# Optimization experiments

Measured on AMD Instinct MI355X. Metric: run time of the kernel, lower is better.

The kernel has to match this reference:

```python
import jax, jax.numpy as jnp
import numpy as np

B, S, D, H = 2, 2048, 768, 12
DK = D // H


def setup_inputs() -> dict:
    key = jax.random.key(0)
    ks = jax.random.split(key, 12)
    inp = {
        "q": jax.random.normal(ks[0], (B, S, D), jnp.float32),
        "k": jax.random.normal(ks[1], (B, S, D), jnp.float32),
        "v": jax.random.normal(ks[2], (B, S, D), jnp.float32),
        # float mask: 1.0 where attention is disallowed (causal upper triangle)
        "mask": (1.0 - jnp.tril(jnp.ones((S, S), jnp.float32)))[None, None],
        "Wq": jax.random.normal(ks[3], (D, D), jnp.float32) / np.sqrt(D),
        "bq": jnp.zeros((D,), jnp.float32),
        "Wk": jax.random.normal(ks[4], (D, D), jnp.float32) / np.sqrt(D),
        "bk": jnp.zeros((D,), jnp.float32),
        "Wv": jax.random.normal(ks[5], (D, D), jnp.float32) / np.sqrt(D),
        "bv": jnp.zeros((D,), jnp.float32),
        "Wo": jax.random.normal(ks[6], (D, D), jnp.float32) / np.sqrt(D),
        "bo": jnp.zeros((D,), jnp.float32),
    }
    return inp


def _split_heads(x):
    # [B,S,D] -> [B,H,S,DK]
    b, s, _ = x.shape
    return x.reshape(b, s, H, DK).transpose(0, 2, 1, 3)


def reference(q, k, v, mask, Wq, bq, Wk, bk, Wv, bv, Wo, bo):
    Q = _split_heads(q @ Wq + bq)
    K = _split_heads(k @ Wk + bk)
    V = _split_heads(v @ Wv + bv)
    scale = jax.lax.rsqrt(jnp.float32(D))  # note: d_model, not d_k (faithful)
    logits = jnp.einsum("bhqd,bhkd->bhqk", Q, K) * scale
    logits = logits + (-1e9) * mask
    weights = jax.nn.softmax(logits, axis=-1)
    attn = jnp.einsum("bhqk,bhkd->bhqd", weights, V)
    attn = attn.transpose(0, 2, 1, 3).reshape(q.shape)  # [B,S,D]
    return jax.nn.relu(attn @ Wo + bo)
```

## Files before the change

### kernel.cpp

```cpp
#include <hip/hip_runtime.h>
#include <math.h>

#define BB 2
#define SS 2048
#define DD 768
#define HH 12
#define DKK 64
#define MM (BB*SS)

typedef _Float16 half_t;
using half8 = __attribute__((ext_vector_type(8))) _Float16;
using half4 = __attribute__((ext_vector_type(4))) _Float16;
using floatx4 = __attribute__((ext_vector_type(4))) float;

__global__ __launch_bounds__(256)
void prep(const float* __restrict__ q, const float* __restrict__ k,
          const float* __restrict__ v,
          const float* __restrict__ Wq, const float* __restrict__ Wk,
          const float* __restrict__ Wv, const float* __restrict__ Wo,
          half_t* __restrict__ qh, half_t* __restrict__ kh,
          half_t* __restrict__ vh,
          half_t* __restrict__ Wqt, half_t* __restrict__ Wkt,
          half_t* __restrict__ Wvt, half_t* __restrict__ Wot)
{
    __shared__ float tile[64][68];
    const int y = blockIdx.y;
    const int t = threadIdx.x;
    if (y < 3) {
        const float* src = y == 0 ? q : (y == 1 ? k : v);
        half_t* dst      = y == 0 ? qh : (y == 1 ? kh : vh);
        int i = blockIdx.x * 256 + t;
        float4 f = ((const float4*)src)[i];
        half4 hv;
        hv[0] = (half_t)f.x; hv[1] = (half_t)f.y;
        hv[2] = (half_t)f.z; hv[3] = (half_t)f.w;
        ((half4*)dst)[i] = hv;
    } else {
        int x = blockIdx.x;
        if (x >= 576) return;
        int w = x / 144, rem = x % 144;
        const float* W = w == 0 ? Wq : w == 1 ? Wk : w == 2 ? Wv : Wo;
        half_t* T      = w == 0 ? Wqt : w == 1 ? Wkt : w == 2 ? Wvt : Wot;
        int k0 = (rem % 12) * 64, n0 = (rem / 12) * 64;
        #pragma unroll
        for (int i = 0; i < 4; ++i) {
            int c = t + i * 256;
            int kr = c >> 4, nc = (c & 15) * 4;
            *(float4*)&tile[kr][nc] = *(const float4*)&W[(size_t)(k0 + kr) * DD + n0 + nc];
        }
        __syncthreads();
        #pragma unroll
        for (int i = 0; i < 4; ++i) {
            int c = t + i * 256;
            int nr = c >> 4, kc = (c & 15) * 4;
            half4 hv;
            #pragma unroll
            for (int jj = 0; jj < 4; ++jj) hv[jj] = (half_t)tile[kc + jj][nr];
            *(half4*)&T[(size_t)(n0 + nr) * DD + k0 + kc] = hv;
        }
    }
}

template<bool SWAP>
__device__ __forceinline__
void gemm_body(const half_t* __restrict__ A, const half_t* __restrict__ Bt,
               floatx4 (&acc)[4][2], half_t (*As)[72], half_t (*Bs)[72],
               int m0, int n0)
{
    const int t = threadIdx.x;
    const int lane = t & 63, wave = t >> 6;
    const int lr = lane & 15, lq = lane >> 4;
    const int wm = (wave >> 1) * 64, wn = (wave & 1) * 32;
    const int a_r = t >> 1,  a_c = (t & 1) * 32;
    const int b_r = t >> 2,  b_c = (t & 3) * 16;

    #pragma unroll
    for (int mi = 0; mi < 4; ++mi)
        #pragma unroll
        for (int ni = 0; ni < 2; ++ni)
            #pragma unroll
            for (int r = 0; r < 4; ++r) acc[mi][ni][r] = 0.f;

    for (int k0 = 0; k0 < DD; k0 += 64) {
        __syncthreads();
        #pragma unroll
        for (int jj = 0; jj < 4; ++jj)
            *(half8*)&As[a_r][a_c + jj * 8] =
                *(const half8*)&A[(size_t)(m0 + a_r) * DD + k0 + a_c + jj * 8];
        #pragma unroll
        for (int jj = 0; jj < 2; ++jj)
            *(half8*)&Bs[b_r][b_c + jj * 8] =
                *(const half8*)&Bt[(size_t)(n0 + b_r) * DD + k0 + b_c + jj * 8];
        __syncthreads();

        half8 af[4][2], bf[2][2];
        #pragma unroll
        for (int mi = 0; mi < 4; ++mi)
            #pragma unroll
            for (int kp = 0; kp < 2; ++kp)
                af[mi][kp] = *(const half8*)&As[wm + mi * 16 + lr][kp * 32 + lq * 8];
        #pragma unroll
        for (int ni = 0; ni < 2; ++ni)
            #pragma unroll
            for (int kp = 0; kp < 2; ++kp)
                bf[ni][kp] = *(const half8*)&Bs[wn + ni * 16 + lr][kp * 32 + lq * 8];

        #pragma unroll
        for (int mi = 0; mi < 4; ++mi)
            #pragma unroll
            for (int ni = 0; ni < 2; ++ni)
                #pragma unroll
                for (int kp = 0; kp < 2; ++kp) {
                    if (SWAP)
                        acc[mi][ni] = __builtin_amdgcn_mfma_f32_16x16x32_f16(
                            bf[ni][kp], af[mi][kp], acc[mi][ni], 0, 0, 0);
                    else
                        acc[mi][ni] = __builtin_amdgcn_mfma_f32_16x16x32_f16(
                            af[mi][kp], bf[ni][kp], acc[mi][ni], 0, 0, 0);
                }
    }
}

__global__ __launch_bounds__(256)
void proj_gemm(const half_t* __restrict__ qh, const half_t* __restrict__ kh,
               const half_t* __restrict__ vh,
               const half_t* __restrict__ Wqt, const half_t* __restrict__ Wkt,
               const half_t* __restrict__ Wvt,
               const float* __restrict__ bq, const float* __restrict__ bk,
               const float* __restrict__ bv,
               half_t* __restrict__ Qo, half_t* __restrict__ Ko,
               half_t* __restrict__ Vto)
{
    const int z = blockIdx.z;
    const half_t* A  = z == 0 ? qh  : z == 1 ? kh  : vh;
    const half_t* Bt = z == 0 ? Wqt : z == 1 ? Wkt : Wvt;
    const float* bias = z == 0 ? bq : z == 1 ? bk : bv;

    __shared__ half_t As[128][72];
    __shared__ half_t Bs[64][72];
    floatx4 acc[4][2];
    const int m0 = blockIdx.y * 128, n0 = blockIdx.x * 64;

    if (z == 2) gemm_body<true >(A, Bt, acc, As, Bs, m0, n0);
    else        gemm_body<false>(A, Bt, acc, As, Bs, m0, n0);

    const int lane = threadIdx.x & 63, wave = threadIdx.x >> 6;
    const int lr = lane & 15, lq = lane >> 4;
    const int wm = (wave >> 1) * 64, wn = (wave & 1) * 32;

    if (z == 2) {
        #pragma unroll
        for (int mi = 0; mi < 4; ++mi)
            #pragma unroll
            for (int ni = 0; ni < 2; ++ni)
                #pragma unroll
                for (int r = 0; r < 4; ++r) {
                    int dcol = n0 + wn + ni * 16 + lq * 4 + r;
                    int srow = m0 + wm + mi * 16 + lr;
                    int hh = dcol >> 6, d = dcol & 63;
                    int b2 = srow >> 11, sdx = srow & 2047;
                    Vto[((size_t)((b2 * HH + hh) * DKK + d)) * SS + sdx] =
                        (half_t)(acc[mi][ni][r] + bias[dcol]);
                }
    } else {
        const float sc = (z == 0) ? 0.03608439182435161f : 1.0f;
        half_t* O = z == 0 ? Qo : Ko;
        #pragma unroll
        for (int mi = 0; mi < 4; ++mi)
            #pragma unroll
            for (int ni = 0; ni < 2; ++ni)
                #pragma unroll
                for (int r = 0; r < 4; ++r) {
                    int row = m0 + wm + mi * 16 + lq * 4 + r;
                    int col = n0 + wn + ni * 16 + lr;
                    O[(size_t)row * DD + col] = (half_t)((acc[mi][ni][r] + bias[col]) * sc);
                }
    }
}

__global__ __launch_bounds__(256)
void out_gemm(const half_t* __restrict__ A, const half_t* __restrict__ Bt,
              const float* __restrict__ bias, float* __restrict__ C)
{
    __shared__ half_t As[128][72];
    __shared__ half_t Bs[64][72];
    floatx4 acc[4][2];
    const int m0 = blockIdx.y * 128, n0 = blockIdx.x * 64;
    gemm_body<false>(A, Bt, acc, As, Bs, m0, n0);

    const int lane = threadIdx.x & 63, wave = threadIdx.x >> 6;
    const int lr = lane & 15, lq = lane >> 4;
    const int wm = (wave >> 1) * 64, wn = (wave & 1) * 32;

    #pragma unroll
    for (int mi = 0; mi < 4; ++mi)
        #pragma unroll
        for (int ni = 0; ni < 2; ++ni)
            #pragma unroll
            for (int r = 0; r < 4; ++r) {
                int row = m0 + wm + mi * 16 + lq * 4 + r;
                int col = n0 + wn + ni * 16 + lr;
                C[(size_t)row * DD + col] = fmaxf(acc[mi][ni][r] + bias[col], 0.f);
            }
}

__device__ const int QT_TAB[40] = {3,4,5,6,7,7,8,8,9,9,10,10,11,11,11,12,12,12,
                                   13,13,13,14,14,14,15,15,15,15,
                                   2,6,10,14, 1,5,9,13, 0,4,8,12};
__device__ const int C_TAB[40]  = {0,0,0,0,0,1,0,1,0,1,0,1,0,1,2,0,1,2,
                                   0,1,2,0,1,2,0,1,2,3,
                                   0,1,2,3, 0,1,2,3, 0,1,2,3};

__global__ __launch_bounds__(256)
void attn_split(const half_t* __restrict__ Qf, const half_t* __restrict__ Kf,
                const half_t* __restrict__ Vt, half_t* __restrict__ Of,
                float* __restrict__ Opart, float* __restrict__ Lpart)
{
    __shared__ half_t Ks[64][72];
    __shared__ half_t Vs[64][72];
    __shared__ half_t Ps[4][32][72];

    const int i = blockIdx.x;
    const int bh = i % 24;
    const int j = i / 24;
    const int qt = QT_TAB[j];
    const int c  = C_TAB[j];
    const bool single = (qt <= 3);
    const int kt0 = c * 8;
    const int iters = 2 * qt + 2;
    const int kt1 = (kt0 + 8 < iters) ? (kt0 + 8) : iters;

    const int b = bh / HH, h = bh % HH;
    const int t = threadIdx.x;
    const int lane = t & 63, wave = t >> 6;
    const int lr = lane & 15, lq = lane >> 4;
    const int q0 = qt * 128;

    const int srow = t >> 3;
    const int scol = (t & 7) * 8;

    const half_t* Kbase = Kf + (size_t)(b * SS) * DD + h * DKK;
    const half_t* Vbase = Vt + (size_t)((b * HH + h) * DKK) * SS;

    half8 kpre[2], vpre[2];
    #pragma unroll
    for (int ii = 0; ii < 2; ++ii) {
        int row = srow + ii * 32;
        kpre[ii] = *(const half8*)&Kbase[(size_t)(kt0 * 64 + row) * DD + scol];
        vpre[ii] = *(const half8*)&Vbase[(size_t)row * SS + kt0 * 64 + scol];
    }

    half8 qa[2][2];
    #pragma unroll
    for (int qg = 0; qg < 2; ++qg) {
        const half_t* qptr =
            Qf + (size_t)(b * SS + q0 + wave * 32 + qg * 16 + lr) * DD + h * DKK;
        qa[qg][0] = *(const half8*)(qptr + lq * 8);
        qa[qg][1] = *(const half8*)(qptr + 32 + lq * 8);
    }

    floatx4 o[2][4];
    #pragma unroll
    for (int qg = 0; qg < 2; ++qg)
        #pragma unroll
        for (int nt = 0; nt < 4; ++nt)
            #pragma unroll
            for (int r = 0; r < 4; ++r) o[qg][nt][r] = 0.f;
    float l_run[2] = {0.f, 0.f};

    for (int kt = kt0; kt < kt1; ++kt) {
        __syncthreads();
        #pragma unroll
        for (int ii = 0; ii < 2; ++ii) {
            int row = srow + ii * 32;
            *(half8*)&Ks[row][scol] = kpre[ii];
            *(half8*)&Vs[row][scol] = vpre[ii];
        }
        __syncthreads();

        if (kt + 1 < kt1) {
            #pragma unroll
            for (int ii = 0; ii < 2; ++ii) {
                int row = srow + ii * 32;
                kpre[ii] = *(const half8*)&Kbase[(size_t)((kt + 1) * 64 + row) * DD + scol];
                vpre[ii] = *(const half8*)&Vbase[(size_t)row * SS + (kt + 1) * 64 + scol];
            }
        }

        floatx4 s[2][4];
        #pragma unroll
        for (int nt = 0; nt < 4; ++nt) {
            half8 kf0 = *(const half8*)&Ks[nt * 16 + lr][lq * 8];
            half8 kf1 = *(const half8*)&Ks[nt * 16 + lr][32 + lq * 8];
            #pragma unroll
            for (int qg = 0; qg < 2; ++qg) {
                floatx4 a = {0.f, 0.f, 0.f, 0.f};
                a = __builtin_amdgcn_mfma_f32_16x16x32_f16(kf0, qa[qg][0], a, 0, 0, 0);
                a = __builtin_amdgcn_mfma_f32_16x16x32_f16(kf1, qa[qg][1], a, 0, 0, 0);
                s[qg][nt] = a;
            }
        }

        if (kt >= 2 * qt) {
            #pragma unroll
            for (int qg = 0; qg < 2; ++qg) {
                int qrow = q0 + wave * 32 + qg * 16 + lr;
                #pragma unroll
                for (int nt = 0; nt < 4; ++nt)
                    #pragma unroll
                    for (int r = 0; r < 4; ++r) {
                        int key = kt * 64 + nt * 16 + lq * 4 + r;
                        if (key > qrow) s[qg][nt][r] = -1e30f;
                    }
            }
        }

        #pragma unroll
        for (int qg = 0; qg < 2; ++qg)
            #pragma unroll
            for (int nt = 0; nt < 4; ++nt) {
                half4 hp;
                #pragma unroll
                for (int r = 0; r < 4; ++r) {
                    float p = __expf(s[qg][nt][r]);
                    l_run[qg] += p;
                    hp[r] = (half_t)p;
                }
                *(half4*)&Ps[wave][qg * 16 + lr][nt * 16 + lq * 4] = hp;
            }

        __builtin_amdgcn_s_waitcnt(0xc07f);

        half8 pa[2][2];
        #pragma unroll
        for (int qg = 0; qg < 2; ++qg) {
            pa[qg][0] = *(const half8*)&Ps[wave][qg * 16 + lr][lq * 8];
            pa[qg][1] = *(const half8*)&Ps[wave][qg * 16 + lr][32 + lq * 8];
        }

        #pragma unroll
        for (int nt = 0; nt < 4; ++nt) {
            half8 vf0 = *(const half8*)&Vs[nt * 16 + lr][lq * 8];
            half8 vf1 = *(const half8*)&Vs[nt * 16 + lr][32 + lq * 8];
            #pragma unroll
            for (int qg = 0; qg < 2; ++qg) {
                o[qg][nt] = __builtin_amdgcn_mfma_f32_16x16x32_f16(vf0, pa[qg][0], o[qg][nt], 0, 0, 0);
                o[qg][nt] = __builtin_amdgcn_mfma_f32_16x16x32_f16(vf1, pa[qg][1], o[qg][nt], 0, 0, 0);
            }
        }
    }

    #pragma unroll
    for (int qg = 0; qg < 2; ++qg) {
        l_run[qg] += __shfl_xor(l_run[qg], 16);
        l_run[qg] += __shfl_xor(l_run[qg], 32);
    }

    if (single) {
        #pragma unroll
        for (int qg = 0; qg < 2; ++qg) {
            float inv = 1.f / l_run[qg];
            int qrow = q0 + wave * 32 + qg * 16 + lr;
            #pragma unroll
            for (int nt = 0; nt < 4; ++nt) {
                half4 hv;
                #pragma unroll
                for (int r = 0; r < 4; ++r) hv[r] = (half_t)(o[qg][nt][r] * inv);
                *(half4*)&Of[(size_t)(b * SS + qrow) * DD + h * DKK + nt * 16 + lq * 4] = hv;
            }
        }
    } else {
        const int p = (bh * 12 + (qt - 4)) * 4 + c;
        float* Ob = Opart + (size_t)p * 8192;
        #pragma unroll
        for (int qg = 0; qg < 2; ++qg) {
            int qq = wave * 32 + qg * 16 + lr;
            #pragma unroll
            for (int nt = 0; nt < 4; ++nt)
                *(floatx4*)&Ob[qq * 64 + nt * 16 + lq * 4] = o[qg][nt];
            if (lq == 0) Lpart[p * 128 + qq] = l_run[qg];
        }
    }
}

__global__ __launch_bounds__(256)
void attn_combine(const float* __restrict__ Opart, const float* __restrict__ Lpart,
                  half_t* __restrict__ Of)
{
    const int ib = blockIdx.x;
    const int bh = ib / 12, qtm = ib % 12;
    const int qt = qtm + 4;
    const int nc = (2 * qt + 9) / 8;
    const int b = bh / HH, h = bh % HH;
    const int pbase = (bh * 12 + qtm) * 4;
    const int t = threadIdx.x;
    const int qq = t >> 1, ds0 = (t & 1) * 32;

    float l = 0.f;
    for (int cc = 0; cc < nc; ++cc) l += Lpart[(pbase + cc) * 128 + qq];
    const float inv = 1.f / l;

    float4 acc[8];
    #pragma unroll
    for (int kk = 0; kk < 8; ++kk) acc[kk] = make_float4(0.f, 0.f, 0.f, 0.f);
    for (int cc = 0; cc < nc; ++cc) {
        const float* Ob = Opart + (size_t)(pbase + cc) * 8192 + qq * 64 + ds0;
        #pragma unroll
        for (int kk = 0; kk < 8; ++kk) {
            float4 x = *(const float4*)&Ob[kk * 4];
            acc[kk].x += x.x; acc[kk].y += x.y; acc[kk].z += x.z; acc[kk].w += x.w;
        }
    }

    int srow = qt * 128 + qq;
    half_t* dst = Of + (size_t)(b * SS + srow) * DD + h * DKK + ds0;
    #pragma unroll
    for (int kk = 0; kk < 8; ++kk) {
        half4 hv;
        hv[0] = (half_t)(acc[kk].x * inv);
        hv[1] = (half_t)(acc[kk].y * inv);
        hv[2] = (half_t)(acc[kk].z * inv);
        hv[3] = (half_t)(acc[kk].w * inv);
        *(half4*)&dst[kk * 4] = hv;
    }
}

extern "C" void kernel_launch(void* const* d_in, const int* in_sizes, int n_in,
                              void* d_out, int out_size, void* d_ws, size_t ws_size,
                              hipStream_t stream)
{
    (void)in_sizes; (void)n_in; (void)out_size; (void)ws_size;
    const float* q  = (const float*)d_in[0];
    const float* k  = (const float*)d_in[1];
    const float* v  = (const float*)d_in[2];
    const float* Wq = (const float*)d_in[4];
    const float* bq = (const float*)d_in[5];
    const float* Wk = (const float*)d_in[6];
    const float* bk = (const float*)d_in[7];
    const float* Wv = (const float*)d_in[8];
    const float* bv = (const float*)d_in[9];
    const float* Wo = (const float*)d_in[10];
    const float* bo = (const float*)d_in[11];
    float* out = (float*)d_out;

    half_t* qh  = (half_t*)d_ws;
    half_t* kh  = qh  + (size_t)MM * DD;
    half_t* vh  = kh  + (size_t)MM * DD;
    half_t* Wqt = vh  + (size_t)MM * DD;
    half_t* Wkt = Wqt + (size_t)DD * DD;
    half_t* Wvt = Wkt + (size_t)DD * DD;
    half_t* Wot = Wvt + (size_t)DD * DD;
    half_t* Qo  = Wot + (size_t)DD * DD;
    half_t* Ko  = Qo  + (size_t)MM * DD;
    half_t* Vto = Ko  + (size_t)MM * DD;
    half_t* Ao  = Vto + (size_t)MM * DD;
    float* Opart = (float*)(Ao + (size_t)MM * DD);
    float* Lpart = Opart + (size_t)1152 * 8192;

    prep<<<dim3(3072, 4), 256, 0, stream>>>(q, k, v, Wq, Wk, Wv, Wo,
                                            qh, kh, vh, Wqt, Wkt, Wvt, Wot);
    proj_gemm<<<dim3(DD / 64, MM / 128, 3), 256, 0, stream>>>(
        qh, kh, vh, Wqt, Wkt, Wvt, bq, bk, bv, Qo, Ko, Vto);
    attn_split<<<dim3(24 * 40), 256, 0, stream>>>(Qo, Ko, Vto, Ao, Opart, Lpart);
    attn_combine<<<dim3(288), 256, 0, stream>>>(Opart, Lpart, Ao);
    out_gemm<<<dim3(DD / 64, MM / 128), 256, 0, stream>>>(Ao, Wot, bo, out);
}
```

Measured before the change: 209.7 us.

## Fuse split-K attention combine via atomic counter, fp16 partials, XCD-aware GEMM tiling

Removes the separate attn_combine kernel. The last split block for each query tile, found with an atomic counter, now does the reduction inline. Partial outputs are stored as fp16 instead of fp32 to halve their traffic, and the GEMM grids are flattened with an XCD-aware block-to-tile mapping so neighbouring M tiles land on the same XCD and share its L2. This adds a memset launch and a threadfence/atomic cost, and the fp16 partials slightly reduce precision.

After: 353.7 us. 1.69x slower.

```diff
diff --git a/kernel.cpp b/kernel.cpp
--- a/kernel.cpp
+++ b/kernel.cpp
@@ -121,6 +121,13 @@
     }
 }
 
+__device__ __forceinline__ void xcd_decode(int bx, int& m0, int& n0)
+{
+    int xcd = bx & 7, g = bx >> 3;
+    m0 = (xcd * 4 + g / 12) * 128;
+    n0 = (g % 12) * 64;
+}
+
 __global__ __launch_bounds__(256)
 void proj_gemm(const half_t* __restrict__ qh, const half_t* __restrict__ kh,
                const half_t* __restrict__ vh,
@@ -139,7 +146,8 @@
     __shared__ half_t As[128][72];
     __shared__ half_t Bs[64][72];
     floatx4 acc[4][2];
-    const int m0 = blockIdx.y * 128, n0 = blockIdx.x * 64;
+    int m0, n0;
+    xcd_decode(blockIdx.x, m0, n0);
 
     if (z == 2) gemm_body<true >(A, Bt, acc, As, Bs, m0, n0);
     else        gemm_body<false>(A, Bt, acc, As, Bs, m0, n0);
@@ -185,7 +193,8 @@
     __shared__ half_t As[128][72];
     __shared__ half_t Bs[64][72];
     floatx4 acc[4][2];
-    const int m0 = blockIdx.y * 128, n0 = blockIdx.x * 64;
+    int m0, n0;
+    xcd_decode(blockIdx.x, m0, n0);
     gemm_body<false>(A, Bt, acc, As, Bs, m0, n0);
 
     const int lane = threadIdx.x & 63, wave = threadIdx.x >> 6;
@@ -214,11 +223,13 @@
 __global__ __launch_bounds__(256)
 void attn_split(const half_t* __restrict__ Qf, const half_t* __restrict__ Kf,
                 const half_t* __restrict__ Vt, half_t* __restrict__ Of,
-                float* __restrict__ Opart, float* __restrict__ Lpart)
+                half_t* __restrict__ Opart, float* __restrict__ Lpart,
+                int* __restrict__ cnt)
 {
     __shared__ half_t Ks[64][72];
     __shared__ half_t Vs[64][72];
     __shared__ half_t Ps[4][32][72];
+    __shared__ int s_last;
 
     const int i = blockIdx.x;
     const int bh = i % 24;
@@ -370,58 +381,59 @@
             }
         }
     } else {
-        const int p = (bh * 12 + (qt - 4)) * 4 + c;
-        float* Ob = Opart + (size_t)p * 8192;
+        const int slot = bh * 12 + (qt - 4);
+        const int p = slot * 4 + c;
+        half_t* Ob = Opart + (size_t)p * 8192;
         #pragma unroll
         for (int qg = 0; qg < 2; ++qg) {
             int qq = wave * 32 + qg * 16 + lr;
             #pragma unroll
-            for (int nt = 0; nt < 4; ++nt)
-                *(floatx4*)&Ob[qq * 64 + nt * 16 + lq * 4] = o[qg][nt];
+            for (int nt = 0; nt < 4; ++nt) {
+                half4 hv;
+                #pragma unroll
+                for (int r = 0; r < 4; ++r) hv[r] = (half_t)o[qg][nt][r];
+                *(half4*)&Ob[qq * 64 + nt * 16 + lq * 4] = hv;
+            }
             if (lq == 0) Lpart[p * 128 + qq] = l_run[qg];
         }
-    }
-}
-
-__global__ __launch_bounds__(256)
-void attn_combine(const float* __restrict__ Opart, const float* __restrict__ Lpart,
-                  half_t* __restrict__ Of)
-{
-    const int ib = blockIdx.x;
-    const int bh = ib / 12, qtm = ib % 12;
-    const int qt = qtm + 4;
-    const int nc = (2 * qt + 9) / 8;
-    const int b = bh / HH, h = bh % HH;
-    const int pbase = (bh * 12 + qtm) * 4;
-    const int t = threadIdx.x;
-    const int qq = t >> 1, ds0 = (t & 1) * 32;
-
-    float l = 0.f;
-    for (int cc = 0; cc < nc; ++cc) l += Lpart[(pbase + cc) * 128 + qq];
-    const float inv = 1.f / l;
-
-    float4 acc[8];
-    #pragma unroll
-    for (int kk = 0; kk < 8; ++kk) acc[kk] = make_float4(0.f, 0.f, 0.f, 0.f);
-    for (int cc = 0; cc < nc; ++cc) {
-        const float* Ob = Opart + (size_t)(pbase + cc) * 8192 + qq * 64 + ds0;
-        #pragma unroll
-        for (int kk = 0; kk < 8; ++kk) {
-            float4 x = *(const float4*)&Ob[kk * 4];
-            acc[kk].x += x.x; acc[kk].y += x.y; acc[kk].z += x.z; acc[kk].w += x.w;
-        }
-    }
-
-    int srow = qt * 128 + qq;
-    half_t* dst = Of + (size_t)(b * SS + srow) * DD + h * DKK + ds0;
-    #pragma unroll
-    for (int kk = 0; kk < 8; ++kk) {
-        half4 hv;
-        hv[0] = (half_t)(acc[kk].x * inv);
-        hv[1] = (half_t)(acc[kk].y * inv);
-        hv[2] = (half_t)(acc[kk].z * inv);
-        hv[3] = (half_t)(acc[kk].w * inv);
-        *(half4*)&dst[kk * 4] = hv;
+
+        __threadfence();
+        __syncthreads();
+        const int nc = (2 * qt + 9) / 8;
+        if (t == 0) {
+            int old = atomicAdd(&cnt[slot], 1);
+            s_last = (old == nc - 1) ? 1 : 0;
+        }
+        __syncthreads();
+        if (s_last) {
+            __threadfence();
+            const int pbase = slot * 4;
+            const int qq = t >> 1, ds0 = (t & 1) * 32;
+            float l = 0.f;
+            for (int cc = 0; cc < nc; ++cc) l += Lpart[(pbase + cc) * 128 + qq];
+            const float inv = 1.f / l;
+            float accv[32];
+            #pragma unroll
+            for (int e = 0; e < 32; ++e) accv[e] = 0.f;
+            for (int cc = 0; cc < nc; ++cc) {
+                const half_t* Os = Opart + (size_t)(pbase + cc) * 8192 + qq * 64 + ds0;
+                #pragma unroll
+                for (int kk = 0; kk < 4; ++kk) {
+                    half8 x = *(const half8*)&Os[kk * 8];
+                    #pragma unroll
+                    for (int e = 0; e < 8; ++e) accv[kk * 8 + e] += (float)x[e];
+                }
+            }
+            int qrow = q0 + qq;
+            half_t* dst = Of + (size_t)(b * SS + qrow) * DD + h * DKK + ds0;
+            #pragma unroll
+            for (int kk = 0; kk < 8; ++kk) {
+                half4 hv;
+                #pragma unroll
+                for (int e = 0; e < 4; ++e) hv[e] = (half_t)(accv[kk * 4 + e] * inv);
+                *(half4*)&dst[kk * 4] = hv;
+            }
+        }
     }
 }
 
@@ -454,14 +466,15 @@
     half_t* Ko  = Qo  + (size_t)MM * DD;
     half_t* Vto = Ko  + (size_t)MM * DD;
     half_t* Ao  = Vto + (size_t)MM * DD;
-    float* Opart = (float*)(Ao + (size_t)MM * DD);
-    float* Lpart = Opart + (size_t)1152 * 8192;
-
+    half_t* Opart = Ao + (size_t)MM * DD;
+    float*  Lpart = (float*)(Opart + (size_t)1152 * 8192);
+    int*    cnt   = (int*)(Lpart + (size_t)1152 * 128);
+
+    hipMemsetAsync(cnt, 0, 288 * sizeof(int), stream);
     prep<<<dim3(3072, 4), 256, 0, stream>>>(q, k, v, Wq, Wk, Wv, Wo,
                                             qh, kh, vh, Wqt, Wkt, Wvt, Wot);
-    proj_gemm<<<dim3(DD / 64, MM / 128, 3), 256, 0, stream>>>(
+    proj_gemm<<<dim3(384, 1, 3), 256, 0, stream>>>(
         qh, kh, vh, Wqt, Wkt, Wvt, bq, bk, bv, Qo, Ko, Vto);
-    attn_split<<<dim3(24 * 40), 256, 0, stream>>>(Qo, Ko, Vto, Ao, Opart, Lpart);
-    attn_combine<<<dim3(288), 256, 0, stream>>>(Opart, Lpart, Ao);
-    out_gemm<<<dim3(DD / 64, MM / 128), 256, 0, stream>>>(Ao, Wot, bo, out);
-}
+    attn_split<<<dim3(24 * 40), 256, 0, stream>>>(Qo, Ko, Vto, Ao, Opart, Lpart, cnt);
+    out_gemm<<<dim3(384), 256, 0, stream>>>(Ao, Wot, bo, out);
+}
```
